# Kernel optimization log

Hardware: AMD Instinct MI355X
Metric: run time of the kernel (lower is better)

The kernel has to match this reference:

```python
import jax, jax.numpy as jnp
import numpy as np

B, L, D = 4, 2048, 2048
S, K, NB = 16, 4, 2
H = D // 64  # num_heads = 32
EPS = 1e-6


def _rms(x, w):
    return x * jax.lax.rsqrt(jnp.mean(x * x, axis=-1, keepdims=True) + EPS) * w


def setup_inputs() -> dict:
    key = jax.random.key(0)
    ks = jax.random.split(key, 8)
    g = lambda k, shape, s: jax.random.normal(k, shape, dtype=jnp.float32) * s
    return {
        'x': g(ks[0], (B, L, D), 1.0),
        'workspace': g(ks[1], (S, D), 0.02),
        'compete_w': g(ks[2], (S, D), 0.02),
        'compete_b': jnp.zeros((S,), jnp.float32),
        'write_w': g(ks[3], (D, D), 0.02),
        'write_b': jnp.zeros((D,), jnp.float32),
        'in_proj_w': g(ks[4], (3 * D, D), 0.02),
        'in_proj_b': jnp.zeros((3 * D,), jnp.float32),
        'out_proj_w': g(ks[5], (D, D), 0.02),
        'out_proj_b': jnp.zeros((D,), jnp.float32),
        'ig_w': g(ks[6], (1, D), 0.02),
        'ig_b': jnp.zeros((1,), jnp.float32),
        'norm_pre_w': jnp.ones((D,), jnp.float32),
        'norm_post_w': jnp.ones((D,), jnp.float32),
    }


def reference(x, workspace, compete_w, compete_b, write_w, write_b,
              in_proj_w, in_proj_b, out_proj_w, out_proj_b,
              ig_w, ig_b, norm_pre_w, norm_post_w):
    Bq, Lq, Dd = x.shape
    hd = Dd // H
    scale = 1.0 / np.sqrt(hd).astype(np.float32)
    ws = jnp.broadcast_to(workspace[None], (Bq, S, Dd))
    wq, wk, wv = in_proj_w[:Dd], in_proj_w[Dd:2 * Dd], in_proj_w[2 * Dd:]
    bq, bk, bv = in_proj_b[:Dd], in_proj_b[Dd:2 * Dd], in_proj_b[2 * Dd:]
    k_eff = min(K, Lq)
    for _ in range(NB):  # n_broadcasts is small & structural
        # slot competition: top-k tokens per slot over the L axis
        logits = _rms(x, norm_pre_w) @ compete_w.T + compete_b       # [B,L,S]
        slot_logits = jnp.swapaxes(logits, 1, 2)                     # [B,S,L]
        vals, idx = jax.lax.top_k(slot_logits, k_eff)                # [B,S,k]
        wgt = jax.nn.softmax(vals, axis=-1)                          # [B,S,k]
        # scatter-softmax + bmm == gather winning tokens and weight-sum
        wx = x @ write_w.T + write_b                                 # [B,L,D]
        gathered = jnp.take_along_axis(wx[:, None], idx[..., None], axis=2)  # [B,S,k,D]
        written = jnp.einsum('bsk,bskd->bsd', wgt, gathered)         # [B,S,D]
        ws = _rms(ws + written, norm_post_w)
        # cross-attention broadcast: tokens query the 16 workspace slots
        q = (x @ wq.T + bq).reshape(Bq, Lq, H, hd)
        kk = (ws @ wk.T + bk).reshape(Bq, S, H, hd)
        vv = (ws @ wv.T + bv).reshape(Bq, S, H, hd)
        att = jax.nn.softmax(jnp.einsum('blhd,bshd->bhls', q, kk) * scale, axis=-1)
        ctx = jnp.einsum('bhls,bshd->blhd', att, vv).reshape(Bq, Lq, Dd)
        x_b = ctx @ out_proj_w.T + out_proj_b
        x = _rms(x + x_b, norm_post_w)
        # ignition head (aux scalar output per token)
        ignition = jax.nn.sigmoid(x @ ig_w.T + ig_b)  # [B,L,1]
    return x
```

## Files before the change

kernel.cpp:

```cpp
#include <hip/hip_runtime.h>
#include <stdint.h>

#define D 2048
#define LSEQ 2048
#define BATCH 4
#define BL (BATCH * LSEQ)
#define NSLOT 16
#define NHEAD 32
#define HDIM 64
#define EPSV 1e-6f

typedef __attribute__((ext_vector_type(8))) short bf16x8;
typedef __attribute__((ext_vector_type(4))) float f32x4;

static __device__ __forceinline__ ushort f2bf(float f) {
    uint32_t u = __float_as_uint(f);
    u += 0x7fffu + ((u >> 16) & 1u);
    return (ushort)(u >> 16);
}

template <int CTRL>
static __device__ __forceinline__ float dpp_xadd(float v) {
    int t = __builtin_amdgcn_mov_dpp(__float_as_int(v), CTRL, 0xf, 0xf, true);
    return v + __int_as_float(t);
}

static __device__ __forceinline__ float wave_sum(float v) {
    v += __shfl_xor(v, 32, 64);
    v += __shfl_xor(v, 16, 64);
    v = dpp_xadd<0x128>(v);
    v += __shfl_xor(v, 4, 64);
    v = dpp_xadd<0x4E>(v);
    v = dpp_xadd<0xB1>(v);
    return v;
}

static __device__ __forceinline__ void gl_lds16(const void* g, void* l) {
    __builtin_amdgcn_global_load_lds(
        (__attribute__((address_space(1))) uint32_t*)(uintptr_t)g,
        (__attribute__((address_space(3))) uint32_t*)(uint32_t)(uintptr_t)l,
        16, 0, 0);
}

__global__ __launch_bounds__(256) void conv_bf16_kernel(const float4* __restrict__ src,
                                                        ushort* __restrict__ dst, int n4) {
    int i = blockIdx.x * 256 + threadIdx.x;
    int stride = gridDim.x * 256;
    for (; i < n4; i += stride) {
        float4 v = src[i];
        uint2 o;
        o.x = (uint)f2bf(v.x) | ((uint)f2bf(v.y) << 16);
        o.y = (uint)f2bf(v.z) | ((uint)f2bf(v.w) << 16);
        *(uint2*)(dst + (size_t)i * 4) = o;
    }
}

__global__ __launch_bounds__(256) void transpose_bf16_kernel(const ushort* __restrict__ src,
                                                             ushort* __restrict__ dst) {
    __shared__ ushort t[64][72];
    int bx = blockIdx.x & 31, by = blockIdx.x >> 5;
    int r0 = by * 64, c0 = bx * 64;
    int tid = threadIdx.x;
    int lr = tid >> 3;
    int lc = (tid & 7) * 8;
#pragma unroll
    for (int p = 0; p < 2; ++p) {
        int rr = p * 32 + lr;
        bf16x8 v = *(const bf16x8*)(src + (size_t)(r0 + rr) * 2048 + c0 + lc);
#pragma unroll
        for (int j = 0; j < 8; ++j) t[lc + j][rr] = (ushort)v[j];
    }
    __syncthreads();
#pragma unroll
    for (int p = 0; p < 2; ++p) {
        int rr = p * 32 + lr;
        *(bf16x8*)(dst + (size_t)(c0 + rr) * 2048 + r0 + lc) = *(const bf16x8*)&t[rr][lc];
    }
}

__global__ __launch_bounds__(256) void logits_kernel(
    const float* __restrict__ x, const float* __restrict__ cw,
    const float* __restrict__ cb, const float* __restrict__ wpre,
    float* __restrict__ logits_t) {
    int blk = blockIdx.x;
    int b = blk >> 9;
    int l0 = (blk & 511) << 2;
    int tid = threadIdx.x;
    int i0 = tid * 8;
    float4 w0 = *(const float4*)(wpre + i0);
    float4 w1 = *(const float4*)(wpre + i0 + 4);
    float wv[8] = {w0.x, w0.y, w0.z, w0.w, w1.x, w1.y, w1.z, w1.w};
    float xw[4][8];
    float ss[4];
#pragma unroll
    for (int r = 0; r < 4; ++r) {
        const float* xr = x + ((size_t)(b * LSEQ + l0 + r)) * D;
        float4 a0 = *(const float4*)(xr + i0);
        float4 a1 = *(const float4*)(xr + i0 + 4);
        float xv[8] = {a0.x, a0.y, a0.z, a0.w, a1.x, a1.y, a1.z, a1.w};
        float s0 = 0.f;
#pragma unroll
        for (int j = 0; j < 8; ++j) { s0 += xv[j] * xv[j]; xw[r][j] = xv[j] * wv[j]; }
        ss[r] = s0;
    }
#pragma unroll
    for (int r = 0; r < 4; ++r) ss[r] = wave_sum(ss[r]);
    __shared__ float red[4][NSLOT][4];
    __shared__ float redss[4][4];
    int lane = tid & 63, w = tid >> 6;
    if (lane == 0) {
#pragma unroll
        for (int r = 0; r < 4; ++r) redss[w][r] = ss[r];
    }
#pragma unroll 2
    for (int s = 0; s < NSLOT; ++s) {
        const float* cwr = cw + (size_t)s * D + i0;
        float4 c0 = *(const float4*)(cwr);
        float4 c1 = *(const float4*)(cwr + 4);
        float acc[4];
#pragma unroll
        for (int r = 0; r < 4; ++r)
            acc[r] = xw[r][0] * c0.x + xw[r][1] * c0.y + xw[r][2] * c0.z + xw[r][3] * c0.w +
                     xw[r][4] * c1.x + xw[r][5] * c1.y + xw[r][6] * c1.z + xw[r][7] * c1.w;
#pragma unroll
        for (int r = 0; r < 4; ++r) acc[r] = wave_sum(acc[r]);
        if (lane == 0) {
#pragma unroll
            for (int r = 0; r < 4; ++r) red[w][s][r] = acc[r];
        }
    }
    __syncthreads();
    if (tid < 64) {
        int s = tid >> 2, r = tid & 3;
        float tot = red[0][s][r] + red[1][s][r] + red[2][s][r] + red[3][s][r];
        float s2 = redss[0][r] + redss[1][r] + redss[2][r] + redss[3][r];
        float rsq = 1.0f / sqrtf(s2 * (1.0f / (float)D) + EPSV);
        logits_t[((size_t)(b * NSLOT + s)) * LSEQ + l0 + r] = tot * rsq + cb[s];
    }
}

__global__ __launch_bounds__(256) void topk_xbar_kernel(
    const float* __restrict__ logits_t, const float* __restrict__ x,
    ushort* __restrict__ xbar_b) {
    int bs = blockIdx.x;
    int b = bs >> 4;
    const float* lr = logits_t + (size_t)bs * LSEQ;
    int tid = threadIdx.x, lane = tid & 63, w = tid >> 6;
    __shared__ float rv[4];
    __shared__ int ri[4];
    __shared__ float selv[4];
    __shared__ int seli[4];
    int i0 = tid * 8;
    float myv[8];
#pragma unroll
    for (int j = 0; j < 8; ++j) myv[j] = lr[i0 + j];
    int chosen[4];
    for (int p = 0; p < 4; ++p) {
        float bv = -3.4e38f;
        int bi = 0x7fffffff;
#pragma unroll
        for (int j = 0; j < 8; ++j) {
            int i = i0 + j;
            bool skip = false;
            for (int q = 0; q < p; ++q) skip = skip || (i == chosen[q]);
            float v = myv[j];
            if (!skip && (v > bv || (v == bv && i < bi))) { bv = v; bi = i; }
        }
#pragma unroll
        for (int off = 1; off < 64; off <<= 1) {
            float ov = __shfl_xor(bv, off, 64);
            int oi = __shfl_xor(bi, off, 64);
            if (ov > bv || (ov == bv && oi < bi)) { bv = ov; bi = oi; }
        }
        if (lane == 0) { rv[w] = bv; ri[w] = bi; }
        __syncthreads();
        if (tid == 0) {
            float fv = rv[0];
            int fi = ri[0];
            for (int q = 1; q < 4; ++q)
                if (rv[q] > fv || (rv[q] == fv && ri[q] < fi)) { fv = rv[q]; fi = ri[q]; }
            selv[p] = fv;
            seli[p] = fi;
        }
        __syncthreads();
        chosen[p] = seli[p];
    }
    float vals[4];
#pragma unroll
    for (int p = 0; p < 4; ++p) vals[p] = selv[p];
    float mx = vals[0];
    float e[4], den = 0.f;
#pragma unroll
    for (int p = 0; p < 4; ++p) { e[p] = expf(vals[p] - mx); den += e[p]; }
    float inv = 1.0f / den;
    const float* xr0 = x + ((size_t)b * LSEQ + chosen[0]) * D;
    const float* xr1 = x + ((size_t)b * LSEQ + chosen[1]) * D;
    const float* xr2 = x + ((size_t)b * LSEQ + chosen[2]) * D;
    const float* xr3 = x + ((size_t)b * LSEQ + chosen[3]) * D;
    float s[8];
#pragma unroll
    for (int j = 0; j < 8; ++j) {
        int i = i0 + j;
        s[j] = (e[0] * xr0[i] + e[1] * xr1[i] + e[2] * xr2[i] + e[3] * xr3[i]) * inv;
    }
    uint4 o;
    o.x = (uint)f2bf(s[0]) | ((uint)f2bf(s[1]) << 16);
    o.y = (uint)f2bf(s[2]) | ((uint)f2bf(s[3]) << 16);
    o.z = (uint)f2bf(s[4]) | ((uint)f2bf(s[5]) << 16);
    o.w = (uint)f2bf(s[6]) | ((uint)f2bf(s[7]) << 16);
    *(uint4*)(xbar_b + (size_t)bs * D + i0) = o;
}

__global__ __launch_bounds__(256) void ws_update_kernel(
    const float* __restrict__ written, const float* __restrict__ ws_prev,
    const float* __restrict__ workspace0, int first,
    const float* __restrict__ wpost, float* __restrict__ ws_out,
    ushort* __restrict__ ws_b) {
    int bs = blockIdx.x;
    int s = bs & (NSLOT - 1);
    int tid = threadIdx.x;
    int i0 = tid * 8;
    const float* prev = first ? (workspace0 + (size_t)s * D) : (ws_prev + (size_t)bs * D);
    const float* wr = written + (size_t)bs * D;
    float4 p0 = *(const float4*)(prev + i0);
    float4 p1 = *(const float4*)(prev + i0 + 4);
    float4 q0 = *(const float4*)(wr + i0);
    float4 q1 = *(const float4*)(wr + i0 + 4);
    float t[8] = {p0.x + q0.x, p0.y + q0.y, p0.z + q0.z, p0.w + q0.w,
                  p1.x + q1.x, p1.y + q1.y, p1.z + q1.z, p1.w + q1.w};
    float ss = 0.f;
#pragma unroll
    for (int j = 0; j < 8; ++j) ss += t[j] * t[j];
    ss = wave_sum(ss);
    __shared__ float sb[4];
    if ((tid & 63) == 0) sb[tid >> 6] = ss;
    __syncthreads();
    ss = sb[0] + sb[1] + sb[2] + sb[3];
    float rsq = 1.0f / sqrtf(ss * (1.0f / (float)D) + EPSV);
    float4 w0 = *(const float4*)(wpost + i0);
    float4 w1 = *(const float4*)(wpost + i0 + 4);
    float wv[8] = {w0.x, w0.y, w0.z, w0.w, w1.x, w1.y, w1.z, w1.w};
    float o[8];
#pragma unroll
    for (int j = 0; j < 8; ++j) o[j] = t[j] * rsq * wv[j];
    float4 r0 = {o[0], o[1], o[2], o[3]};
    float4 r1 = {o[4], o[5], o[6], o[7]};
    *(float4*)(ws_out + (size_t)bs * D + i0) = r0;
    *(float4*)(ws_out + (size_t)bs * D + i0 + 4) = r1;
    uint4 ob;
    ob.x = (uint)f2bf(o[0]) | ((uint)f2bf(o[1]) << 16);
    ob.y = (uint)f2bf(o[2]) | ((uint)f2bf(o[3]) << 16);
    ob.z = (uint)f2bf(o[4]) | ((uint)f2bf(o[5]) << 16);
    ob.w = (uint)f2bf(o[6]) | ((uint)f2bf(o[7]) << 16);
    *(uint4*)(ws_b + (size_t)bs * D + i0) = ob;
}

__global__ __launch_bounds__(256) void resid_rms_kernel(
    const float* __restrict__ x_src, const ushort* __restrict__ ao,
    const float* __restrict__ wpost, float* __restrict__ x_dst,
    ushort* __restrict__ xb) {
    int row = blockIdx.x;
    int tid = threadIdx.x;
    int i0 = tid * 8;
    const float* xr = x_src + (size_t)row * D;
    uint4 av = *(const uint4*)(ao + (size_t)row * D + i0);
    float af[8];
    af[0] = __uint_as_float(av.x << 16);
    af[1] = __uint_as_float(av.x & 0xffff0000u);
    af[2] = __uint_as_float(av.y << 16);
    af[3] = __uint_as_float(av.y & 0xffff0000u);
    af[4] = __uint_as_float(av.z << 16);
    af[5] = __uint_as_float(av.z & 0xffff0000u);
    af[6] = __uint_as_float(av.w << 16);
    af[7] = __uint_as_float(av.w & 0xffff0000u);
    float4 p0 = *(const float4*)(xr + i0);
    float4 p1 = *(const float4*)(xr + i0 + 4);
    float t[8] = {p0.x + af[0], p0.y + af[1], p0.z + af[2], p0.w + af[3],
                  p1.x + af[4], p1.y + af[5], p1.z + af[6], p1.w + af[7]};
    float ss = 0.f;
#pragma unroll
    for (int j = 0; j < 8; ++j) ss += t[j] * t[j];
    ss = wave_sum(ss);
    __shared__ float sb[4];
    if ((tid & 63) == 0) sb[tid >> 6] = ss;
    __syncthreads();
    ss = sb[0] + sb[1] + sb[2] + sb[3];
    float rsq = 1.0f / sqrtf(ss * (1.0f / (float)D) + EPSV);
    float4 w0 = *(const float4*)(wpost + i0);
    float4 w1 = *(const float4*)(wpost + i0 + 4);
    float wv[8] = {w0.x, w0.y, w0.z, w0.w, w1.x, w1.y, w1.z, w1.w};
    float o[8];
#pragma unroll
    for (int j = 0; j < 8; ++j) o[j] = t[j] * rsq * wv[j];
    float4 r0 = {o[0], o[1], o[2], o[3]};
    float4 r1 = {o[4], o[5], o[6], o[7]};
    *(float4*)(x_dst + (size_t)row * D + i0) = r0;
    *(float4*)(x_dst + (size_t)row * D + i0 + 4) = r1;
    uint4 ob;
    ob.x = (uint)f2bf(o[0]) | ((uint)f2bf(o[1]) << 16);
    ob.y = (uint)f2bf(o[2]) | ((uint)f2bf(o[3]) << 16);
    ob.z = (uint)f2bf(o[4]) | ((uint)f2bf(o[5]) << 16);
    ob.w = (uint)f2bf(o[6]) | ((uint)f2bf(o[7]) << 16);
    *(uint4*)(xb + (size_t)row * D + i0) = ob;
}

template <int TRANS>
static __device__ __forceinline__ void grouped16_body(
    int blk, const ushort* __restrict__ Abase, const ushort* __restrict__ Bmat,
    ushort* __restrict__ Cout) {
    int g = blk >> 3;
    int nt = blk & 7;
    int h = g & 31;
    int hoff = h * 64;
    int tid = threadIdx.x, lane = tid & 63, wv = tid >> 6;
    int j0 = nt * 256 + wv * 64;
    int rr = lane & 15, ko = lane >> 4;
    const ushort* A = Abase + (size_t)g * 16 * 64;
    bf16x8 af0 = *(const bf16x8*)(A + rr * 64 + ko * 8);
    bf16x8 af1 = *(const bf16x8*)(A + rr * 64 + 32 + ko * 8);
    f32x4 acc[4];
    f32x4 zero = {0.f, 0.f, 0.f, 0.f};
#pragma unroll
    for (int nf = 0; nf < 4; ++nf) acc[nf] = zero;
#pragma unroll
    for (int nf = 0; nf < 4; ++nf) {
        int j = j0 + nf * 16 + rr;
        bf16x8 b0 = *(const bf16x8*)(Bmat + (size_t)j * 2048 + hoff + ko * 8);
        bf16x8 b1 = *(const bf16x8*)(Bmat + (size_t)j * 2048 + hoff + 32 + ko * 8);
        acc[nf] = __builtin_amdgcn_mfma_f32_16x16x32_bf16(af0, b0, acc[nf], 0, 0, 0);
        acc[nf] = __builtin_amdgcn_mfma_f32_16x16x32_bf16(af1, b1, acc[nf], 0, 0, 0);
    }
#pragma unroll
    for (int nf = 0; nf < 4; ++nf)
#pragma unroll
        for (int r = 0; r < 4; ++r) {
            int s = ko * 4 + r;
            int j = j0 + nf * 16 + rr;
            ushort v = f2bf(acc[nf][r]);
            if (TRANS) Cout[(size_t)j * 2048 + g * 16 + s] = v;
            else       Cout[(size_t)(g * 16 + s) * 2048 + j] = v;
        }
}

__global__ __launch_bounds__(256) void fused_prep_kernel(
    const ushort* __restrict__ kb16, const ushort* __restrict__ vb16,
    const float* __restrict__ bq, const ushort* __restrict__ wqt,
    const ushort* __restrict__ wob, ushort* __restrict__ ktil,
    ushort* __restrict__ wtilT, float* __restrict__ cbias) {
    int blk = blockIdx.x;
    if (blk < 1024) {
        grouped16_body<0>(blk, kb16, wqt, ktil);
    } else if (blk < 2048) {
        grouped16_body<1>(blk - 1024, vb16, wob, wtilT);
    } else {
        int i = (blk - 2048) * 256 + threadIdx.x;
        int hs = i & 511;
        int h = hs >> 4;
        const ushort* kr = kb16 + (size_t)i * 64;
        const float* bb = bq + h * 64;
        float acc = 0.f;
#pragma unroll
        for (int d = 0; d < 64; ++d)
            acc += __uint_as_float(((uint)kr[d]) << 16) * bb[d];
        cbias[i] = acc;
    }
}

__global__ __launch_bounds__(256) void attn_sm_kernel(
    const ushort* __restrict__ qlog, const float* __restrict__ cb,
    ushort* __restrict__ aatt) {
    int blk = blockIdx.x;
    int tid = threadIdx.x;
    int l = blk * 8 + (tid >> 5);
    int b = l >> 11;
    int h = tid & 31;
    const ushort* q0 = qlog + (size_t)l * 512 + h * 16;
    const ushort* q1 = q0 + (size_t)BL * 512;
    const float* c = cb + b * 512 + h * 16;
    uint4 u0a = *(const uint4*)q0;
    uint4 u0b = *(const uint4*)(q0 + 8);
    uint4 u1a = *(const uint4*)q1;
    uint4 u1b = *(const uint4*)(q1 + 8);
    uint ua[8] = {u0a.x, u0a.y, u0a.z, u0a.w, u0b.x, u0b.y, u0b.z, u0b.w};
    uint ub[8] = {u1a.x, u1a.y, u1a.z, u1a.w, u1b.x, u1b.y, u1b.z, u1b.w};
    float p[16];
#pragma unroll
    for (int i = 0; i < 8; ++i) {
        float a0 = __uint_as_float(ua[i] << 16);
        float a1 = __uint_as_float(ua[i] & 0xffff0000u);
        float b0 = __uint_as_float(ub[i] << 16);
        float b1 = __uint_as_float(ub[i] & 0xffff0000u);
        p[2 * i]     = a0 + b0 + c[2 * i];
        p[2 * i + 1] = a1 + b1 + c[2 * i + 1];
    }
    float mx = p[0];
#pragma unroll
    for (int s = 1; s < 16; ++s) mx = fmaxf(mx, p[s]);
    float den = 0.f;
#pragma unroll
    for (int s = 0; s < 16; ++s) { p[s] = __expf((p[s] - mx) * 0.125f); den += p[s]; }
    float inv = 1.0f / den;
    uint4 o[2];
    uint* ow = (uint*)o;
#pragma unroll
    for (int i = 0; i < 8; ++i)
        ow[i] = (uint)f2bf(p[2 * i] * inv) | ((uint)f2bf(p[2 * i + 1] * inv) << 16);
    ushort* dst = aatt + (size_t)l * 512 + h * 16;
    *(uint4*)dst = o[0];
    *(uint4*)(dst + 8) = o[1];
}

template <int KVMODE>
__global__ __launch_bounds__(256) void gemm_tiny(
    const ushort* __restrict__ A, const ushort* __restrict__ Bw,
    const float* __restrict__ bias, float* __restrict__ C,
    int M, int N, int K, ushort* __restrict__ kvk, ushort* __restrict__ kvv) {
    int gw = (blockIdx.x * 256 + threadIdx.x) >> 6;
    int lane = threadIdx.x & 63;
    int ntiles = N >> 4;
    int nt = gw % ntiles, mt = gw / ntiles;
    int rr = lane & 15, ko = lane >> 4;
    const ushort* Ar = A + (size_t)(mt * 16 + rr) * K;
    const ushort* Br = Bw + (size_t)(nt * 16 + rr) * K;
    f32x4 acc = {0.f, 0.f, 0.f, 0.f};
    int NT = K / 32;
#pragma unroll 8
    for (int t = 0; t < NT; ++t) {
        bf16x8 af = *(const bf16x8*)(Ar + t * 32 + ko * 8);
        bf16x8 bf = *(const bf16x8*)(Br + t * 32 + ko * 8);
        acc = __builtin_amdgcn_mfma_f32_16x16x32_bf16(af, bf, acc, 0, 0, 0);
    }
    int col = nt * 16 + rr;
    float bsv = bias ? bias[col] : 0.f;
#pragma unroll
    for (int r = 0; r < 4; ++r) {
        int rowi = mt * 16 + ko * 4 + r;
        float v = acc[r] + bsv;
        if (KVMODE) {
            int b = rowi >> 4, s = rowi & 15;
            int c2 = (col < 2048) ? col : col - 2048;
            int h = c2 >> 6, d = c2 & 63;
            size_t dst = (((size_t)(b * NHEAD + h)) * NSLOT + s) * HDIM + d;
            if (col < 2048) kvk[dst] = f2bf(v);
            else            kvv[dst] = f2bf(v);
        } else {
            C[(size_t)rowi * N + col] = v;
        }
    }
}

template <int BM, int OBF>
__global__ __launch_bounds__(256) void gemm_bt(
    const ushort* __restrict__ A, const ushort* __restrict__ Bw,
    const float* __restrict__ bias, float* __restrict__ C,
    int M, int N, int K, size_t bOff, int bStride, int aStride,
    int zA, int zB, size_t zC, int ntz) {
    constexpr int BN = 128, BK = 32;
    constexpr int MF = BM / 32;
    constexpr int APASS = (BM * BK / 8) / 256;
    __shared__ short lds[2][(BM + BN) * BK];
    int tid = threadIdx.x;
    int lane = tid & 63, w = tid >> 6;
    int wr = w >> 1, wc = w & 1;
    int ntx = N / BN;
    int total = gridDim.x;
    int per = total >> 3;
    int xcd = blockIdx.x & 7;
    int j = blockIdx.x >> 3;
    int pairs_per = per / ntx;
    int pair = xcd * pairs_per + j / ntx;
    int bx = j % ntx;
    int by = pair / ntz;
    int ksl = pair % ntz;
    int tn = bx * BN;
    int tm = by * BM;
    A += (size_t)ksl * zA;
    Bw += (size_t)ksl * zB + (size_t)(tm >> 11) * bOff;
    C += (size_t)ksl * zC;
    f32x4 acc[MF][4];
    f32x4 zero = {0.f, 0.f, 0.f, 0.f};
#pragma unroll
    for (int m = 0; m < MF; ++m)
#pragma unroll
        for (int n = 0; n < 4; ++n) acc[m][n] = zero;
    int NT = K / BK;

    auto stage = [&](int buf, int t) {
        int kt = t * BK;
#pragma unroll
        for (int p = 0; p < APASS; ++p) {
            int cb = p * 256 + w * 64;
            int c = cb + lane;
            int L = c >> 3, slot = c & 7;
            int lc = slot ^ (L & 7);
            int r = 2 * L + (lc >> 2);
            int k8 = (lc & 3) * 8;
            int gr = tm + r;
            if (gr >= M) gr = M - 1;
            gl_lds16(A + (size_t)gr * aStride + kt + k8, (void*)&lds[buf][cb * 8]);
        }
#pragma unroll
        for (int p = 0; p < 2; ++p) {
            int cb = p * 256 + w * 64;
            int c = cb + lane;
            int L = c >> 3, slot = c & 7;
            int lc = slot ^ (L & 7);
            int r = 2 * L + (lc >> 2);
            int k8 = (lc & 3) * 8;
            gl_lds16(Bw + (size_t)(tn + r) * bStride + kt + k8,
                     (void*)&lds[buf][BM * BK + cb * 8]);
        }
    };
    stage(0, 0);
    for (int t = 0; t < NT; ++t) {
        __syncthreads();
        if (t + 1 < NT) stage((t + 1) & 1, t + 1);
        const short* Ab = &lds[t & 1][0];
        const short* Bb = &lds[t & 1][BM * BK];
        int kc = lane >> 4;
        int rr = lane & 15;
        bf16x8 af[MF], bfr[4];
#pragma unroll
        for (int m = 0; m < MF; ++m) {
            int row = wr * (MF * 16) + m * 16 + rr;
            int L = row >> 1;
            int sl = (((row & 1) * 4 + kc)) ^ (L & 7);
            af[m] = *(const bf16x8*)&Ab[L * 64 + sl * 8];
        }
#pragma unroll
        for (int n = 0; n < 4; ++n) {
            int row = wc * 64 + n * 16 + rr;
            int L = row >> 1;
            int sl = (((row & 1) * 4 + kc)) ^ (L & 7);
            bfr[n] = *(const bf16x8*)&Bb[L * 64 + sl * 8];
        }
#pragma unroll
        for (int m = 0; m < MF; ++m)
#pragma unroll
            for (int n = 0; n < 4; ++n)
                acc[m][n] = __builtin_amdgcn_mfma_f32_16x16x32_bf16(af[m], bfr[n],
                                                                    acc[m][n], 0, 0, 0);
    }
#pragma unroll
    for (int m = 0; m < MF; ++m) {
#pragma unroll
        for (int n = 0; n < 4; ++n) {
            int col = tn + wc * 64 + n * 16 + (lane & 15);
            float bsv = bias ? bias[col] : 0.f;
#pragma unroll
            for (int r = 0; r < 4; ++r) {
                int rowi = tm + wr * (MF * 16) + m * 16 + (lane >> 4) * 4 + r;
                if (rowi >= M) continue;
                float v = acc[m][n][r] + bsv;
                if (OBF) ((ushort*)C)[(size_t)rowi * N + col] = f2bf(v);
                else     C[(size_t)rowi * N + col] = v;
            }
        }
    }
}

extern "C" void kernel_launch(void* const* d_in, const int* in_sizes, int n_in,
                              void* d_out, int out_size, void* d_ws, size_t ws_size,
                              hipStream_t stream) {
    const float* x_in       = (const float*)d_in[0];
    const float* workspace  = (const float*)d_in[1];
    const float* compete_w  = (const float*)d_in[2];
    const float* compete_b  = (const float*)d_in[3];
    const float* write_w    = (const float*)d_in[4];
    const float* write_b    = (const float*)d_in[5];
    const float* in_proj_w  = (const float*)d_in[6];
    const float* in_proj_b  = (const float*)d_in[7];
    const float* out_proj_w = (const float*)d_in[8];
    const float* out_proj_b = (const float*)d_in[9];
    const float* norm_pre_w  = (const float*)d_in[12];
    const float* norm_post_w = (const float*)d_in[13];
    float* xout = (float*)d_out;

    char* base = (char*)d_ws;
    size_t off = 0;
    auto alloc = [&](size_t bytes) {
        void* p = base + off;
        off += (bytes + 255) & ~(size_t)255;
        return p;
    };
    ushort* xb      = (ushort*)alloc((size_t)BL * D * 2);
    ushort* xbb     = (ushort*)alloc((size_t)BL * D * 2);
    float*  logits  = (float*) alloc((size_t)BATCH * NSLOT * LSEQ * 4);
    ushort* xbar    = (ushort*)alloc((size_t)BATCH * NSLOT * D * 2);
    float*  written = (float*) alloc((size_t)BATCH * NSLOT * D * 4);
    float*  wsbuf   = (float*) alloc((size_t)BATCH * NSLOT * D * 4);
    ushort* wsb     = (ushort*)alloc((size_t)BATCH * NSLOT * D * 2);
    ushort* ipb     = (ushort*)alloc((size_t)3 * D * D * 2);
    ushort* wob     = (ushort*)alloc((size_t)D * D * 2);
    ushort* wwb     = (ushort*)alloc((size_t)D * D * 2);
    ushort* wqt     = (ushort*)alloc((size_t)D * D * 2);
    ushort* kb16    = (ushort*)alloc((size_t)BATCH * NHEAD * NSLOT * HDIM * 2);
    ushort* vb16    = (ushort*)alloc((size_t)BATCH * NHEAD * NSLOT * HDIM * 2);
    ushort* ktil    = (ushort*)alloc((size_t)BATCH * 512 * D * 2);
    ushort* wtilT   = (ushort*)alloc((size_t)D * BATCH * 512 * 2);
    ushort* qlogb   = (ushort*)alloc((size_t)2 * BL * 512 * 2);
    ushort* aatt    = (ushort*)alloc((size_t)BL * 512 * 2);
    float*  cbias   = (float*) alloc((size_t)BATCH * 512 * 4);
    (void)ws_size; (void)in_sizes; (void)n_in; (void)out_size;

    conv_bf16_kernel<<<2048, 256, 0, stream>>>((const float4*)in_proj_w, ipb, 3 * D * D / 4);
    conv_bf16_kernel<<<2048, 256, 0, stream>>>((const float4*)out_proj_w, wob, D * D / 4);
    conv_bf16_kernel<<<2048, 256, 0, stream>>>((const float4*)write_w, wwb, D * D / 4);
    conv_bf16_kernel<<<2048, 256, 0, stream>>>((const float4*)x_in, xb, BL * D / 4);
    transpose_bf16_kernel<<<1024, 256, 0, stream>>>(ipb, wqt);

    for (int it = 0; it < 2; ++it) {
        const float* xs = it ? (const float*)xout : x_in;
        logits_kernel<<<BL / 4, 256, 0, stream>>>(xs, compete_w, compete_b, norm_pre_w,
                                                  logits);
        topk_xbar_kernel<<<BATCH * NSLOT, 256, 0, stream>>>(logits, xs, xbar);
        gemm_tiny<0><<<128, 256, 0, stream>>>(xbar, wwb, write_b, written,
                                              BATCH * NSLOT, D, D,
                                              (ushort*)nullptr, (ushort*)nullptr);
        ws_update_kernel<<<BATCH * NSLOT, 256, 0, stream>>>(written, wsbuf, workspace,
                                                            it == 0 ? 1 : 0, norm_post_w,
                                                            wsbuf, wsb);
        gemm_tiny<1><<<256, 256, 0, stream>>>(wsb, ipb + (size_t)D * D, in_proj_b + D,
                                              (float*)nullptr, BATCH * NSLOT, 2 * D, D,
                                              kb16, vb16);
        fused_prep_kernel<<<2056, 256, 0, stream>>>(kb16, vb16, in_proj_b, wqt, wob,
                                                    ktil, wtilT, cbias);
        gemm_bt<64, 1><<<1024, 256, 0, stream>>>(
            xb, ktil, (const float*)nullptr, (float*)qlogb, BL, 512, D / 2,
            (size_t)512 * D, D, D, D / 2, D / 2, (size_t)(BL * 512 / 2), 2);
        attn_sm_kernel<<<BL / 8, 256, 0, stream>>>(qlogb, cbias, aatt);
        gemm_bt<64, 1><<<2048, 256, 0, stream>>>(
            aatt, wtilT, out_proj_b, (float*)xbb, BL, D, 512,
            (size_t)512, D, 512, 0, 0, 0, 1);
        resid_rms_kernel<<<BL, 256, 0, stream>>>(xs, xbb, norm_post_w, xout, xb);
    }
}
```

Baseline: 481.3 us.

## Fuse query-logit GEMM with per-head softmax, dropping split-K intermediate

Replaces the split-K GEMM that wrote two bf16 partial logit buffers, and the separate softmax kernel, with one GEMM that runs the full K=2048 reduction and applies the 16-slot softmax in the epilogue using cross-lane shuffles. This removes the qlogb round trip through memory and one kernel launch. In exchange the grid shrinks from 1024 to 512 blocks with a longer K loop each, which may lower occupancy and parallelism. The epilogue also writes scattered 2-byte stores.

```diff
diff --git a/kernel.cpp b/kernel.cpp
--- a/kernel.cpp
+++ b/kernel.cpp
@@ -32,6 +32,21 @@
     v += __shfl_xor(v, 4, 64);
     v = dpp_xadd<0x4E>(v);
     v = dpp_xadd<0xB1>(v);
+    return v;
+}
+
+static __device__ __forceinline__ float grp16_max(float v) {
+    v = fmaxf(v, __shfl_xor(v, 1, 64));
+    v = fmaxf(v, __shfl_xor(v, 2, 64));
+    v = fmaxf(v, __shfl_xor(v, 4, 64));
+    v = fmaxf(v, __shfl_xor(v, 8, 64));
+    return v;
+}
+static __device__ __forceinline__ float grp16_sum(float v) {
+    v += __shfl_xor(v, 1, 64);
+    v += __shfl_xor(v, 2, 64);
+    v += __shfl_xor(v, 4, 64);
+    v += __shfl_xor(v, 8, 64);
     return v;
 }
 
@@ -366,50 +381,6 @@
     }
 }
 
-__global__ __launch_bounds__(256) void attn_sm_kernel(
-    const ushort* __restrict__ qlog, const float* __restrict__ cb,
-    ushort* __restrict__ aatt) {
-    int blk = blockIdx.x;
-    int tid = threadIdx.x;
-    int l = blk * 8 + (tid >> 5);
-    int b = l >> 11;
-    int h = tid & 31;
-    const ushort* q0 = qlog + (size_t)l * 512 + h * 16;
-    const ushort* q1 = q0 + (size_t)BL * 512;
-    const float* c = cb + b * 512 + h * 16;
-    uint4 u0a = *(const uint4*)q0;
-    uint4 u0b = *(const uint4*)(q0 + 8);
-    uint4 u1a = *(const uint4*)q1;
-    uint4 u1b = *(const uint4*)(q1 + 8);
-    uint ua[8] = {u0a.x, u0a.y, u0a.z, u0a.w, u0b.x, u0b.y, u0b.z, u0b.w};
-    uint ub[8] = {u1a.x, u1a.y, u1a.z, u1a.w, u1b.x, u1b.y, u1b.z, u1b.w};
-    float p[16];
-#pragma unroll
-    for (int i = 0; i < 8; ++i) {
-        float a0 = __uint_as_float(ua[i] << 16);
-        float a1 = __uint_as_float(ua[i] & 0xffff0000u);
-        float b0 = __uint_as_float(ub[i] << 16);
-        float b1 = __uint_as_float(ub[i] & 0xffff0000u);
-        p[2 * i]     = a0 + b0 + c[2 * i];
-        p[2 * i + 1] = a1 + b1 + c[2 * i + 1];
-    }
-    float mx = p[0];
-#pragma unroll
-    for (int s = 1; s < 16; ++s) mx = fmaxf(mx, p[s]);
-    float den = 0.f;
-#pragma unroll
-    for (int s = 0; s < 16; ++s) { p[s] = __expf((p[s] - mx) * 0.125f); den += p[s]; }
-    float inv = 1.0f / den;
-    uint4 o[2];
-    uint* ow = (uint*)o;
-#pragma unroll
-    for (int i = 0; i < 8; ++i)
-        ow[i] = (uint)f2bf(p[2 * i] * inv) | ((uint)f2bf(p[2 * i + 1] * inv) << 16);
-    ushort* dst = aatt + (size_t)l * 512 + h * 16;
-    *(uint4*)dst = o[0];
-    *(uint4*)(dst + 8) = o[1];
-}
-
 template <int KVMODE>
 __global__ __launch_bounds__(256) void gemm_tiny(
     const ushort* __restrict__ A, const ushort* __restrict__ Bw,
@@ -445,6 +416,104 @@
             else            kvv[dst] = f2bf(v);
         } else {
             C[(size_t)rowi * N + col] = v;
+        }
+    }
+}
+
+__global__ __launch_bounds__(256) void gemm_qsm_kernel(
+    const ushort* __restrict__ A, const ushort* __restrict__ ktil,
+    const float* __restrict__ cbias, ushort* __restrict__ aatt) {
+    constexpr int BM = 64, BN = 128, BK = 32;
+    constexpr int MF = 2;
+    __shared__ short lds[2][(BM + BN) * BK];
+    int tid = threadIdx.x;
+    int lane = tid & 63, w = tid >> 6;
+    int wr = w >> 1, wc = w & 1;
+    int xcd = blockIdx.x & 7;
+    int j = blockIdx.x >> 3;
+    int by = xcd * 16 + (j >> 2);
+    int bx = j & 3;
+    int tn = bx * BN;
+    int tm = by * BM;
+    int b = tm >> 11;
+    const ushort* Bw = ktil + (size_t)b * 512 * D;
+    f32x4 acc[MF][4];
+    f32x4 zero = {0.f, 0.f, 0.f, 0.f};
+#pragma unroll
+    for (int m = 0; m < MF; ++m)
+#pragma unroll
+        for (int n = 0; n < 4; ++n) acc[m][n] = zero;
+    int NT = D / BK;
+
+    auto stage = [&](int buf, int t) {
+        int kt = t * BK;
+        {
+            int cb = w * 64;
+            int c = cb + lane;
+            int L = c >> 3, slot = c & 7;
+            int lc = slot ^ (L & 7);
+            int r = 2 * L + (lc >> 2);
+            int k8 = (lc & 3) * 8;
+            gl_lds16(A + (size_t)(tm + r) * D + kt + k8, (void*)&lds[buf][cb * 8]);
+        }
+#pragma unroll
+        for (int p = 0; p < 2; ++p) {
+            int cb = p * 256 + w * 64;
+            int c = cb + lane;
+            int L = c >> 3, slot = c & 7;
+            int lc = slot ^ (L & 7);
+            int r = 2 * L + (lc >> 2);
+            int k8 = (lc & 3) * 8;
+            gl_lds16(Bw + (size_t)(tn + r) * D + kt + k8,
+                     (void*)&lds[buf][BM * BK + cb * 8]);
+        }
+    };
+    stage(0, 0);
+    for (int t = 0; t < NT; ++t) {
+        __syncthreads();
+        if (t + 1 < NT) stage((t + 1) & 1, t + 1);
+        const short* Ab = &lds[t & 1][0];
+        const short* Bb = &lds[t & 1][BM * BK];
+        int kc = lane >> 4;
+        int rr = lane & 15;
+        bf16x8 af[MF], bfr[4];
+#pragma unroll
+        for (int m = 0; m < MF; ++m) {
+            int row = wr * (MF * 16) + m * 16 + rr;
+            int L = row >> 1;
+            int sl = (((row & 1) * 4 + kc)) ^ (L & 7);
+            af[m] = *(const bf16x8*)&Ab[L * 64 + sl * 8];
+        }
+#pragma unroll
+        for (int n = 0; n < 4; ++n) {
+            int row = wc * 64 + n * 16 + rr;
+            int L = row >> 1;
+            int sl = (((row & 1) * 4 + kc)) ^ (L & 7);
+            bfr[n] = *(const bf16x8*)&Bb[L * 64 + sl * 8];
+        }
+#pragma unroll
+        for (int m = 0; m < MF; ++m)
+#pragma unroll
+            for (int n = 0; n < 4; ++n)
+                acc[m][n] = __builtin_amdgcn_mfma_f32_16x16x32_bf16(af[m], bfr[n],
+                                                                    acc[m][n], 0, 0, 0);
+    }
+    int rr = lane & 15, ko = lane >> 4;
+#pragma unroll
+    for (int n = 0; n < 4; ++n) {
+        int col = tn + wc * 64 + n * 16 + rr;
+        float cbv = cbias[b * 512 + col];
+#pragma unroll
+        for (int m = 0; m < MF; ++m) {
+#pragma unroll
+            for (int r = 0; r < 4; ++r) {
+                float p = acc[m][n][r] + cbv;
+                float mx = grp16_max(p);
+                float e = __expf((p - mx) * 0.125f);
+                float den = grp16_sum(e);
+                int row = tm + wr * (MF * 16) + m * 16 + ko * 4 + r;
+                aatt[(size_t)row * 512 + col] = f2bf(e / den);
+            }
         }
     }
 }
@@ -598,7 +667,6 @@
     ushort* vb16    = (ushort*)alloc((size_t)BATCH * NHEAD * NSLOT * HDIM * 2);
     ushort* ktil    = (ushort*)alloc((size_t)BATCH * 512 * D * 2);
     ushort* wtilT   = (ushort*)alloc((size_t)D * BATCH * 512 * 2);
-    ushort* qlogb   = (ushort*)alloc((size_t)2 * BL * 512 * 2);
     ushort* aatt    = (ushort*)alloc((size_t)BL * 512 * 2);
     float*  cbias   = (float*) alloc((size_t)BATCH * 512 * 4);
     (void)ws_size; (void)in_sizes; (void)n_in; (void)out_size;
@@ -625,10 +693,7 @@
                                               kb16, vb16);
         fused_prep_kernel<<<2056, 256, 0, stream>>>(kb16, vb16, in_proj_b, wqt, wob,
                                                     ktil, wtilT, cbias);
-        gemm_bt<64, 1><<<1024, 256, 0, stream>>>(
-            xb, ktil, (const float*)nullptr, (float*)qlogb, BL, 512, D / 2,
-            (size_t)512 * D, D, D, D / 2, D / 2, (size_t)(BL * 512 / 2), 2);
-        attn_sm_kernel<<<BL / 8, 256, 0, stream>>>(qlogb, cbias, aatt);
+        gemm_qsm_kernel<<<512, 256, 0, stream>>>(xb, ktil, cbias, aatt);
         gemm_bt<64, 1><<<2048, 256, 0, stream>>>(
             aatt, wtilT, out_proj_b, (float*)xbb, BL, D, 512,
             (size_t)512, D, 512, 0, 0, 0, 1);
```

Result: faster. 453.6 us (-5.8%).
